# Kernel optimization log

Hardware: AMD Instinct MI355X
Metric: run time of the kernel (lower is better)

## Reference

```python
import jax, jax.numpy as jnp
import numpy as np

N = 20000
E = 100000
IN_CH = 512
OUT_CH = 256
HID = 2 * OUT_CH          # 512
CAT = 5 * HID             # 2560
BN_EPS = 1e-5


def _sage(x, src, dst, w_edge, Wl, Wr, b):
    """PyG SAGEConv (mean aggr): lin_l(mean_{j->i} x_j) + lin_r(x_i).
    w_edge: per-edge float weight (0/1 mask); messages flow src -> dst."""
    msg = x[src] * w_edge[:, None]                              # [E, F]
    s = jax.ops.segment_sum(msg, dst, num_segments=N)           # [N, F]
    cnt = jax.ops.segment_sum(w_edge, dst, num_segments=N)      # [N]
    mean = s / jnp.maximum(cnt, 1.0)[:, None]
    return mean @ Wl.T + x @ Wr.T + b


def setup_inputs() -> dict:
    key = jax.random.key(0)
    ks = jax.random.split(key, 12)
    x = jax.random.normal(ks[0], (N, IN_CH), dtype=jnp.float32)
    edge_index = jax.random.randint(ks[1], (2, E), 0, N, dtype=jnp.int64)
    edge_attr = jax.random.randint(ks[2], (E,), 0, 5, dtype=jnp.int64)
    sc = 1.0 / np.sqrt(IN_CH)
    Wl5 = jax.random.uniform(ks[3], (5, HID, IN_CH), jnp.float32, -sc, sc)
    Wr5 = jax.random.uniform(ks[4], (5, HID, IN_CH), jnp.float32, -sc, sc)
    bl5 = jnp.zeros((5, HID), jnp.float32)
    sc2 = 1.0 / np.sqrt(CAT)
    Wmu_l = jax.random.uniform(ks[5], (OUT_CH, CAT), jnp.float32, -sc2, sc2)
    Wmu_r = jax.random.uniform(ks[6], (OUT_CH, CAT), jnp.float32, -sc2, sc2)
    bmu = jnp.zeros((OUT_CH,), jnp.float32)
    Wlv_l = jax.random.uniform(ks[7], (OUT_CH, CAT), jnp.float32, -sc2, sc2)
    Wlv_r = jax.random.uniform(ks[8], (OUT_CH, CAT), jnp.float32, -sc2, sc2)
    blv = jnp.zeros((OUT_CH,), jnp.float32)
    gamma = jnp.ones((CAT,), jnp.float32)
    beta = jnp.zeros((CAT,), jnp.float32)
    run_mean = jax.random.normal(ks[9], (CAT,), jnp.float32) * 0.1
    run_var = jnp.abs(jax.random.normal(ks[10], (CAT,), jnp.float32)) + 1.0
    return {"x": x, "edge_index": edge_index, "edge_attr": edge_attr,
            "Wl5": Wl5, "Wr5": Wr5, "bl5": bl5,
            "Wmu_l": Wmu_l, "Wmu_r": Wmu_r, "bmu": bmu,
            "Wlv_l": Wlv_l, "Wlv_r": Wlv_r, "blv": blv,
            "gamma": gamma, "beta": beta,
            "run_mean": run_mean, "run_var": run_var}


def reference(x, edge_index, edge_attr, Wl5, Wr5, bl5,
              Wmu_l, Wmu_r, bmu, Wlv_l, Wlv_r, blv,
              gamma, beta, run_mean, run_var):
    # eval mode: all dropouts are identity, BatchNorm uses running stats.
    src, dst = edge_index[0], edge_index[1]
    # 5 relation branches: mask edges by relation id instead of nonzero slicing
    branches = []
    for k in range(5):
        w = (edge_attr == k).astype(x.dtype)                    # [E]
        h = _sage(x, src, dst, w, Wl5[k], Wr5[k], bl5[k])       # [N, HID]
        branches.append(jax.nn.relu(h))
    h = jnp.concatenate(branches, axis=1)                       # [N, CAT]
    # BatchNorm1d (eval)
    h = (h - run_mean) * jax.lax.rsqrt(run_var + BN_EPS) * gamma + beta
    ones = jnp.ones((E,), x.dtype)
    mu = _sage(h, src, dst, ones, Wmu_l, Wmu_r, bmu)            # [N, OUT_CH]
    logvar = _sage(h, src, dst, ones, Wlv_l, Wlv_r, blv)        # [N, OUT_CH]
    return (mu, logvar)
```

## Files before the change

kernel.cpp:

```cpp
#include <hip/hip_runtime.h>
#include <stdint.h>

#define INCH 512
#define HIDW 512
#define CATW 2560
#define OUTW 256
#define BN_EPS 1e-5f
#define TS 1024

typedef __bf16 bf16x8 __attribute__((ext_vector_type(8)));
typedef float f32x4 __attribute__((ext_vector_type(4)));

__device__ __forceinline__ unsigned short f2bf(float f) {
  union { float f; unsigned u; } v; v.f = f;
  unsigned r = v.u + 0x7FFFu + ((v.u >> 16) & 1u);
  return (unsigned short)(r >> 16);
}

__device__ __forceinline__ float bf2f(unsigned short u) {
  union { unsigned u; float f; } v; v.u = ((unsigned)u) << 16; return v.f;
}

__device__ __forceinline__ void pack4(unsigned short* dst, float a, float b, float c, float d) {
  unsigned lo = (unsigned)f2bf(a) | ((unsigned)f2bf(b) << 16);
  unsigned hi = (unsigned)f2bf(c) | ((unsigned)f2bf(d) << 16);
  *reinterpret_cast<uint2*>(dst) = make_uint2(lo, hi);
}


__global__ void cvt_bf16_kernel(const float* __restrict__ in, unsigned short* __restrict__ out, int n4) {
  int g = blockIdx.x * blockDim.x + threadIdx.x;
  if (g >= n4) return;
  int base = g * 4;
  float4 v = *reinterpret_cast<const float4*>(in + base);
  pack4(out + base, v.x, v.y, v.z, v.w);
}

__global__ void pack_w1p_kernel(const float* __restrict__ Wl, const float* __restrict__ Wr,
                                unsigned short* __restrict__ out) {
  int g = blockIdx.x * blockDim.x + threadIdx.x;
  if (g >= 5 * 128 * 512) return;
  int z = g >> 16;
  int rem = g & 65535;
  int c = rem >> 9;
  int j = rem & 511;
  int kk = c * 8;
  const float* src = (kk < 512) ? (Wl + ((size_t)(z * 512 + j)) * 512 + kk)
                                : (Wr + ((size_t)(z * 512 + j)) * 512 + (kk - 512));
  float4 a = *reinterpret_cast<const float4*>(src);
  float4 b = *reinterpret_cast<const float4*>(src + 4);
  pack4(out + (size_t)g * 8, a.x, a.y, a.z, a.w);
  pack4(out + (size_t)g * 8 + 4, b.x, b.y, b.z, b.w);
}

__global__ void pack_w23p_kernel(const float* __restrict__ Wmu_l, const float* __restrict__ Wlv_l,
                                 const float* __restrict__ Wmu_r, const float* __restrict__ Wlv_r,
                                 unsigned short* __restrict__ out) {
  int g = blockIdx.x * blockDim.x + threadIdx.x;
  if (g >= 320 * 1024) return;
  int c = g >> 10;
  int j = g & 1023;
  const float* row;
  if (j < 256)       row = Wmu_l + (size_t)j * CATW;
  else if (j < 512)  row = Wlv_l + (size_t)(j - 256) * CATW;
  else if (j < 768)  row = Wmu_r + (size_t)(j - 512) * CATW;
  else               row = Wlv_r + (size_t)(j - 768) * CATW;
  const float* src = row + c * 8;
  float4 a = *reinterpret_cast<const float4*>(src);
  float4 b = *reinterpret_cast<const float4*>(src + 4);
  pack4(out + (size_t)g * 8, a.x, a.y, a.z, a.w);
  pack4(out + (size_t)g * 8 + 4, b.x, b.y, b.z, b.w);
}


__global__ void hist_kernel(const int* __restrict__ ei, const int* __restrict__ ea,
                            int* __restrict__ cnt, int E) {
  int e = blockIdx.x * 256 + threadIdx.x;
  if (e >= E) return;
  atomicAdd(&cnt[ei[E + e] * 5 + ea[e]], 1);
}

__global__ void scan1_kernel(const int* __restrict__ in, int* __restrict__ out,
                             int* __restrict__ bsum, int n) {
  __shared__ int lds[256];
  int t = threadIdx.x;
  int base = blockIdx.x * TS + t * 4;
  int4 v = make_int4(0, 0, 0, 0);
  if (base + 3 < n) v = *reinterpret_cast<const int4*>(in + base);
  else {
    if (base < n) v.x = in[base];
    if (base + 1 < n) v.y = in[base + 1];
    if (base + 2 < n) v.z = in[base + 2];
    if (base + 3 < n) v.w = in[base + 3];
  }
  int s = v.x + v.y + v.z + v.w;
  lds[t] = s;
  __syncthreads();
  for (int o = 1; o < 256; o <<= 1) {
    int a = (t >= o) ? lds[t - o] : 0;
    __syncthreads();
    lds[t] += a;
    __syncthreads();
  }
  int excl = lds[t] - s;
  if (t == 255) bsum[blockIdx.x] = lds[255];
  int e0 = excl, e1 = e0 + v.x, e2 = e1 + v.y, e3 = e2 + v.z;
  if (base < n) out[base] = e0;
  if (base + 1 < n) out[base + 1] = e1;
  if (base + 2 < n) out[base + 2] = e2;
  if (base + 3 < n) out[base + 3] = e3;
}

__global__ void scan2_kernel(int* __restrict__ bsum, int nb) {
  __shared__ int lds[128];
  int t = threadIdx.x;
  int v = (t < nb) ? bsum[t] : 0;
  lds[t] = v;
  __syncthreads();
  for (int o = 1; o < 128; o <<= 1) {
    int a = (t >= o) ? lds[t - o] : 0;
    __syncthreads();
    lds[t] += a;
    __syncthreads();
  }
  if (t < nb) bsum[t] = lds[t] - v;
}

__global__ void scan3_kernel(int* __restrict__ out, const int* __restrict__ bsum,
                             int n, int total) {
  int g = blockIdx.x * 256 + threadIdx.x;
  if (g == 0) out[n] = total;
  int base = g * 4;
  if (base >= n) return;
  int add = bsum[base / TS];
  if (base + 3 < n) {
    int4 v = *reinterpret_cast<int4*>(out + base);
    v.x += add; v.y += add; v.z += add; v.w += add;
    *reinterpret_cast<int4*>(out + base) = v;
  } else {
    for (int q = 0; q < 4 && base + q < n; ++q) out[base + q] += add;
  }
}

__global__ void fill_kernel(const int* __restrict__ ei, const int* __restrict__ ea,
                            const int* __restrict__ offs, int* __restrict__ fillc,
                            int* __restrict__ perm, int E) {
  int e = blockIdx.x * 256 + threadIdx.x;
  if (e >= E) return;
  int key = ei[E + e] * 5 + ea[e];
  int p = atomicAdd(&fillc[key], 1);
  perm[offs[key] + p] = ei[e];
}


__global__ void gather1_kernel(const unsigned short* __restrict__ xb, const int* __restrict__ offs,
                               const int* __restrict__ perm, unsigned short* __restrict__ meanb5) {
  int i = blockIdx.x;
  int k = blockIdx.y;
  int t = threadIdx.x;
  int b0 = offs[i * 5 + k], b1 = offs[i * 5 + k + 1];
  float a0 = 0.f, a1 = 0.f, a2 = 0.f, a3 = 0.f;
  for (int e = b0; e < b1; ++e) {
    int s = perm[e];
    ushort4 v = reinterpret_cast<const ushort4*>(xb + (size_t)s * 512)[t];
    a0 += bf2f(v.x); a1 += bf2f(v.y); a2 += bf2f(v.z); a3 += bf2f(v.w);
  }
  float inv = (b1 > b0) ? 1.0f / (float)(b1 - b0) : 0.0f;
  pack4(meanb5 + (size_t)i * CATW + k * 512 + t * 4, a0 * inv, a1 * inv, a2 * inv, a3 * inv);
}

__global__ void gather2_kernel(const float* __restrict__ z, const int* __restrict__ offs,
                               const int* __restrict__ perm, float* __restrict__ mean2) {
  int i = blockIdx.x;
  int t = threadIdx.x;
  int b0 = offs[i * 5], b1 = offs[i * 5 + 5];
  float4 acc = make_float4(0.f, 0.f, 0.f, 0.f);
  for (int e = b0; e < b1; ++e) {
    int s = perm[e];
    float4 v = reinterpret_cast<const float4*>(z + (size_t)s * 512)[t];
    acc.x += v.x; acc.y += v.y; acc.z += v.z; acc.w += v.w;
  }
  float inv = (b1 > b0) ? 1.0f / (float)(b1 - b0) : 1.0f;
  reinterpret_cast<float4*>(mean2 + (size_t)i * 512)[t] =
      make_float4(acc.x * inv, acc.y * inv, acc.z * inv, acc.w * inv);
}

__global__ void add_kernel(float* __restrict__ dout, const float* __restrict__ mean2,
                           const float* __restrict__ bmu, const float* __restrict__ blv,
                           int M, int n4) {
  int g = blockIdx.x * 256 + threadIdx.x;
  if (g >= n4) return;
  int base = g * 4;
  int i = base >> 9;
  int c = base & 511;
  float4 m2 = *reinterpret_cast<const float4*>(mean2 + (size_t)i * 512 + c);
  int cc = c & 255;
  float* op;
  const float* bp;
  if (c < 256) { op = dout + (size_t)i * OUTW + cc; bp = bmu + cc; }
  else         { op = dout + (size_t)M * OUTW + (size_t)i * OUTW + cc; bp = blv + cc; }
  float4 y = *reinterpret_cast<float4*>(op);
  float4 b = *reinterpret_cast<const float4*>(bp);
  y.x += m2.x + b.x; y.y += m2.y + b.y; y.z += m2.z + b.z; y.w += m2.w + b.w;
  *reinterpret_cast<float4*>(op) = y;
}

template<int MODE>
__global__ __launch_bounds__(256, 3)
void gemm_kernel(const unsigned short* __restrict__ A,
                 const unsigned short* __restrict__ A2,
                 const unsigned short* __restrict__ B,
                 unsigned short* __restrict__ hOut,
                 float* __restrict__ fOut,
                 float* __restrict__ fOut2,
                 const float* __restrict__ p0,
                 const float* __restrict__ p1,
                 const float* __restrict__ p2,
                 const float* __restrict__ p3,
                 const float* __restrict__ p4,
                 int M)
{
  constexpr int KTOT = (MODE == 0) ? (2 * INCH) : CATW;
  constexpr int KT = KTOT / 32;
  constexpr int NBLK = (MODE == 0) ? 4 : 8;
  constexpr int NC = (MODE == 0) ? 512 : 1024;

  const int nwg = gridDim.x;
  const int o = blockIdx.x;
  const int q = nwg >> 3, r = nwg & 7;
  const int xcd = o & 7;
  const int wg = (xcd < r ? xcd * (q + 1) : r * (q + 1) + (xcd - r) * q) + (o >> 3);
  const int rowBase = (wg / NBLK) * 128;
  const int nBase = (wg % NBLK) * 128;
  const int z = (MODE == 0) ? blockIdx.z : 0;
  const unsigned short* BpF = (MODE == 0) ? (B + (size_t)z * 524288) : B;

  __shared__ unsigned short As[4][4096];

  const int tid = threadIdx.x;
  const int lane = tid & 63;
  const int wv = tid >> 6;
  const int wr = wv >> 1, wc = wv & 1;
  const int lr = lane & 15, kg = lane >> 4;

  const int srow0 = (wv * 2) * 16 + (lane >> 2);
  const int srow1 = srow0 + 16;
  const int kswz = (((lane & 3) ^ ((lane >> 4) & 3)) * 8);
  int gar0 = rowBase + srow0; if (gar0 >= M) gar0 = M - 1;
  int gar1 = rowBase + srow1; if (gar1 >= M) gar1 = M - 1;

  int aslot[4];
#pragma unroll
  for (int m = 0; m < 4; ++m) {
    const int ar = wr * 64 + m * 16 + lr;
    aslot[m] = ar * 32 + ((kg ^ ((lr >> 2) & 3)) * 8);
  }

  size_t bjoff[4];
#pragma unroll
  for (int n = 0; n < 4; ++n)
    bjoff[n] = (size_t)(nBase + wc * 64 + n * 16 + lr) * 8;

  f32x4 acc[4][4] = {};

  auto stageA = [&](int slot, int kt) {
    const int kk0 = kt * 32;
    const unsigned short *a0p, *a1p;
    if (MODE == 0) {
      if (kk0 < INCH) {
        a0p = A + (size_t)gar0 * CATW + z * 512 + kk0 + kswz;
        a1p = A + (size_t)gar1 * CATW + z * 512 + kk0 + kswz;
      } else {
        a0p = A2 + (size_t)gar0 * INCH + (kk0 - INCH) + kswz;
        a1p = A2 + (size_t)gar1 * INCH + (kk0 - INCH) + kswz;
      }
    } else {
      a0p = A + (size_t)gar0 * KTOT + kk0 + kswz;
      a1p = A + (size_t)gar1 * KTOT + kk0 + kswz;
    }
    __builtin_amdgcn_global_load_lds((const void*)a0p, (void*)&As[slot][(wv * 2) * 512], 16, 0, 0);
    __builtin_amdgcn_global_load_lds((const void*)a1p, (void*)&As[slot][(wv * 2 + 1) * 512], 16, 0, 0);
  };

  auto loadB = [&](int kt, bf16x8 (&dst)[4]) {
    const size_t cbase = (size_t)((kt << 2) + kg) * NC * 8;
#pragma unroll
    for (int n = 0; n < 4; ++n)
      dst[n] = *reinterpret_cast<const bf16x8*>(BpF + cbase + bjoff[n]);
  };

  auto step = [&](int t, const bf16x8 (&bcur)[4], bf16x8 (&bnxt)[4]) {
    const int slot = t & 3;
    bf16x8 af[4];
#pragma unroll
    for (int m = 0; m < 4; ++m)
      af[m] = *reinterpret_cast<const bf16x8*>(&As[slot][aslot[m]]);
    if (t + 1 < KT) loadB(t + 1, bnxt);
    if (t + 3 < KT) stageA((t + 3) & 3, t + 3);
    __builtin_amdgcn_sched_barrier(0);
    __builtin_amdgcn_s_setprio(1);
#pragma unroll
    for (int m = 0; m < 4; ++m)
#pragma unroll
      for (int n = 0; n < 4; ++n)
        acc[m][n] = __builtin_amdgcn_mfma_f32_16x16x32_bf16(af[m], bcur[n], acc[m][n], 0, 0, 0);
    __builtin_amdgcn_s_setprio(0);
    __builtin_amdgcn_sched_barrier(0);
    __builtin_amdgcn_s_barrier();
    __builtin_amdgcn_sched_barrier(0);
  };

  bf16x8 bP[4], bQ[4];
  stageA(0, 0);
  stageA(1, 1);
  stageA(2, 2);
  __builtin_amdgcn_sched_barrier(0);
  loadB(0, bP);
  __builtin_amdgcn_sched_barrier(0);
  asm volatile("s_waitcnt vmcnt(8)" ::: "memory");
  __builtin_amdgcn_s_barrier();
  __builtin_amdgcn_sched_barrier(0);

  for (int t = 0; t < KT; t += 2) {
    step(t, bP, bQ);
    step(t + 1, bQ, bP);
  }

#pragma unroll
  for (int n = 0; n < 4; ++n) {
    const int j = nBase + wc * 64 + n * 16 + lr;
    if (MODE == 0) {
      const int ch = z * 512 + j;
      const float bias = p0[ch];
      const float scale = rsqrtf(p2[ch] + BN_EPS) * p3[ch];
      const float rm = p1[ch], be = p4[ch];
#pragma unroll
      for (int m = 0; m < 4; ++m) {
        const int ib = rowBase + wr * 64 + m * 16 + kg * 4;
#pragma unroll
        for (int rr = 0; rr < 4; ++rr) {
          const int i = ib + rr;
          if (i < M) {
            float v = acc[m][n][rr] + bias;
            v = fmaxf(v, 0.0f);
            v = (v - rm) * scale + be;
            hOut[(size_t)i * CATW + ch] = f2bf(v);
          }
        }
      }
    } else {
#pragma unroll
      for (int m = 0; m < 4; ++m) {
        const int ib = rowBase + wr * 64 + m * 16 + kg * 4;
#pragma unroll
        for (int rr = 0; rr < 4; ++rr) {
          const int i = ib + rr;
          if (i < M) {
            const float v = acc[m][n][rr];
            if (j < 512) {
              fOut[(size_t)i * 512 + j] = v;
            } else {
              const int jj = j - 512;
              size_t o2 = (jj < OUTW) ? ((size_t)i * OUTW + jj)
                                      : ((size_t)M * OUTW + (size_t)i * OUTW + (jj - OUTW));
              fOut2[o2] = v;
            }
          }
        }
      }
    }
  }
}


extern "C" void kernel_launch(void* const* d_in, const int* in_sizes, int n_in,
                              void* d_out, int out_size, void* d_ws, size_t ws_size,
                              hipStream_t stream) {
  const float* x     = (const float*)d_in[0];
  const int*   ei    = (const int*)d_in[1];
  const int*   ea    = (const int*)d_in[2];
  const float* Wl5   = (const float*)d_in[3];
  const float* Wr5   = (const float*)d_in[4];
  const float* bl5   = (const float*)d_in[5];
  const float* Wmu_l = (const float*)d_in[6];
  const float* Wmu_r = (const float*)d_in[7];
  const float* bmu   = (const float*)d_in[8];
  const float* Wlv_l = (const float*)d_in[9];
  const float* Wlv_r = (const float*)d_in[10];
  const float* blv   = (const float*)d_in[11];
  const float* gamma = (const float*)d_in[12];
  const float* beta  = (const float*)d_in[13];
  const float* rmean = (const float*)d_in[14];
  const float* rvar  = (const float*)d_in[15];
  (void)n_in; (void)out_size;

  const int N = in_sizes[0] / INCH;
  const int E = in_sizes[2];
  const int NKEY = N * 5;

  char* ws = (char*)d_ws;
  size_t off = 0;
  auto take = [&](size_t bytes) { char* p = ws + off; off += (bytes + 255) & ~(size_t)255; return p; };
  unsigned short* hb = (unsigned short*)take((size_t)N * CATW * 2);
  char* U = take((size_t)N * CATW * 2);
  unsigned short* xb = (unsigned short*)take((size_t)N * 512 * 2);
  unsigned short* w1p  = (unsigned short*)take((size_t)5 * 128 * 512 * 8 * 2);
  unsigned short* w23p = (unsigned short*)take((size_t)320 * 1024 * 8 * 2);
  int* cntk  = (int*)take((size_t)NKEY * 4);
  int* offs  = (int*)take((size_t)(NKEY + 1) * 4);
  int* fillc = (int*)take((size_t)NKEY * 4);
  int* perm  = (int*)take((size_t)E * 4);
  int* bsum  = (int*)take(256 * 4);
  if (off > ws_size) return;

  unsigned short* meanb5 = (unsigned short*)U;
  float* zbuf  = (float*)U;
  float* mean2 = (float*)(U + (size_t)N * 512 * 4);

  cvt_bf16_kernel<<<dim3((N * INCH / 4 + 255) / 256), 256, 0, stream>>>(x, xb, N * INCH / 4);
  pack_w1p_kernel<<<dim3((5 * 128 * 512 + 255) / 256), 256, 0, stream>>>(Wl5, Wr5, w1p);
  pack_w23p_kernel<<<dim3((320 * 1024 + 255) / 256), 256, 0, stream>>>(Wmu_l, Wlv_l, Wmu_r, Wlv_r, w23p);

  hipMemsetAsync(cntk, 0, (size_t)NKEY * 4, stream);
  hipMemsetAsync(fillc, 0, (size_t)NKEY * 4, stream);
  hist_kernel<<<dim3((E + 255) / 256), 256, 0, stream>>>(ei, ea, cntk, E);
  const int nb = (NKEY + TS - 1) / TS;
  scan1_kernel<<<dim3(nb), 256, 0, stream>>>(cntk, offs, bsum, NKEY);
  scan2_kernel<<<dim3(1), 128, 0, stream>>>(bsum, nb);
  scan3_kernel<<<dim3((NKEY / 4 + 255) / 256 + 1), 256, 0, stream>>>(offs, bsum, NKEY, E);
  fill_kernel<<<dim3((E + 255) / 256), 256, 0, stream>>>(ei, ea, offs, fillc, perm, E);

  gather1_kernel<<<dim3(N, 5), 128, 0, stream>>>(xb, offs, perm, meanb5);
  const int mblk = (N + 127) / 128;
  gemm_kernel<0><<<dim3(mblk * 4, 1, 5), 256, 0, stream>>>(
      meanb5, xb, w1p, hb, nullptr, nullptr,
      bl5, rmean, rvar, gamma, beta, N);

  gemm_kernel<1><<<dim3(mblk * 8, 1, 1), 256, 0, stream>>>(
      hb, nullptr, w23p, nullptr, zbuf, (float*)d_out,
      nullptr, nullptr, nullptr, nullptr, nullptr, N);

  gather2_kernel<<<dim3(N), 128, 0, stream>>>(zbuf, offs, perm, mean2);

  add_kernel<<<dim3((N * 512 / 4 + 255) / 256), 256, 0, stream>>>(
      (float*)d_out, mean2, bmu, blv, N, N * 512 / 4);
}
```

Measured before the change: 435.8 us.

## Stage GEMM epilogues through LDS for coalesced stores and fuse add into gather2

Both GEMM epilogues now write accumulator tiles into shared memory (swizzled for the bf16 path) and then emit 16-byte vectorized, row-contiguous global stores, replacing scattered 2- and 4-byte stores. The second gather kernel now adds the neighbor mean plus bias directly into the output, which removes the separate add kernel and the intermediate mean2 buffer round-trip. The cost is extra LDS traffic and barriers in the epilogue, plus reuse of the A staging buffer, which must be large enough for 128x128 bf16 or 128x64 fp32 tiles.

```diff
diff --git a/kernel.cpp b/kernel.cpp
--- a/kernel.cpp
+++ b/kernel.cpp
@@ -170,7 +170,9 @@
 }
 
 __global__ void gather2_kernel(const float* __restrict__ z, const int* __restrict__ offs,
-                               const int* __restrict__ perm, float* __restrict__ mean2) {
+                               const int* __restrict__ perm, float* __restrict__ dout,
+                               const float* __restrict__ bmu, const float* __restrict__ blv,
+                               int M) {
   int i = blockIdx.x;
   int t = threadIdx.x;
   int b0 = offs[i * 5], b1 = offs[i * 5 + 5];
@@ -181,27 +183,15 @@
     acc.x += v.x; acc.y += v.y; acc.z += v.z; acc.w += v.w;
   }
   float inv = (b1 > b0) ? 1.0f / (float)(b1 - b0) : 1.0f;
-  reinterpret_cast<float4*>(mean2 + (size_t)i * 512)[t] =
-      make_float4(acc.x * inv, acc.y * inv, acc.z * inv, acc.w * inv);
-}
-
-__global__ void add_kernel(float* __restrict__ dout, const float* __restrict__ mean2,
-                           const float* __restrict__ bmu, const float* __restrict__ blv,
-                           int M, int n4) {
-  int g = blockIdx.x * 256 + threadIdx.x;
-  if (g >= n4) return;
-  int base = g * 4;
-  int i = base >> 9;
-  int c = base & 511;
-  float4 m2 = *reinterpret_cast<const float4*>(mean2 + (size_t)i * 512 + c);
-  int cc = c & 255;
+  int c = t * 4;
   float* op;
   const float* bp;
-  if (c < 256) { op = dout + (size_t)i * OUTW + cc; bp = bmu + cc; }
-  else         { op = dout + (size_t)M * OUTW + (size_t)i * OUTW + cc; bp = blv + cc; }
+  if (c < 256) { op = dout + (size_t)i * OUTW + c; bp = bmu + c; }
+  else         { op = dout + (size_t)M * OUTW + (size_t)i * OUTW + (c - 256); bp = blv + (c - 256); }
   float4 y = *reinterpret_cast<float4*>(op);
   float4 b = *reinterpret_cast<const float4*>(bp);
-  y.x += m2.x + b.x; y.y += m2.y + b.y; y.z += m2.z + b.z; y.w += m2.w + b.w;
+  y.x += acc.x * inv + b.x; y.y += acc.y * inv + b.y;
+  y.z += acc.z * inv + b.z; y.w += acc.w * inv + b.w;
   *reinterpret_cast<float4*>(op) = y;
 }
 
@@ -326,46 +316,76 @@
     step(t + 1, bQ, bP);
   }
 
-#pragma unroll
-  for (int n = 0; n < 4; ++n) {
-    const int j = nBase + wc * 64 + n * 16 + lr;
-    if (MODE == 0) {
-      const int ch = z * 512 + j;
+  if (MODE == 0) {
+    unsigned short* lds16 = &As[0][0];
+#pragma unroll
+    for (int n = 0; n < 4; ++n) {
+      const int j = wc * 64 + n * 16 + lr;
+      const int ch = z * 512 + nBase + j;
       const float bias = p0[ch];
       const float scale = rsqrtf(p2[ch] + BN_EPS) * p3[ch];
       const float rm = p1[ch], be = p4[ch];
 #pragma unroll
-      for (int m = 0; m < 4; ++m) {
-        const int ib = rowBase + wr * 64 + m * 16 + kg * 4;
+      for (int m = 0; m < 4; ++m)
 #pragma unroll
         for (int rr = 0; rr < 4; ++rr) {
-          const int i = ib + rr;
-          if (i < M) {
-            float v = acc[m][n][rr] + bias;
-            v = fmaxf(v, 0.0f);
-            v = (v - rm) * scale + be;
-            hOut[(size_t)i * CATW + ch] = f2bf(v);
-          }
+          const int row = wr * 64 + m * 16 + kg * 4 + rr;
+          float v = acc[m][n][rr] + bias;
+          v = fmaxf(v, 0.0f);
+          v = (v - rm) * scale + be;
+          lds16[row * 128 + (j ^ ((row & 7) << 3))] = f2bf(v);
+        }
+    }
+    __syncthreads();
+    const int trow = tid >> 4;
+    const int cb = tid & 15;
+#pragma unroll
+    for (int p = 0; p < 8; ++p) {
+      const int row = p * 16 + trow;
+      const int i = rowBase + row;
+      if (i < M) {
+        const int scb = cb ^ (row & 7);
+        uint4 v = *reinterpret_cast<const uint4*>(&lds16[row * 128 + scb * 8]);
+        *reinterpret_cast<uint4*>(&hOut[(size_t)i * CATW + z * 512 + nBase + cb * 8]) = v;
+      }
+    }
+  } else {
+    float* ldsf = reinterpret_cast<float*>(&As[0][0]);
+#pragma unroll
+    for (int hp = 0; hp < 2; ++hp) {
+      __syncthreads();
+      if (wc == hp) {
+#pragma unroll
+        for (int n = 0; n < 4; ++n) {
+          const int jl = n * 16 + lr;
+#pragma unroll
+          for (int m = 0; m < 4; ++m)
+#pragma unroll
+            for (int rr = 0; rr < 4; ++rr) {
+              const int row = wr * 64 + m * 16 + kg * 4 + rr;
+              ldsf[row * 64 + jl] = acc[m][n][rr];
+            }
         }
       }
-    } else {
-#pragma unroll
-      for (int m = 0; m < 4; ++m) {
-        const int ib = rowBase + wr * 64 + m * 16 + kg * 4;
-#pragma unroll
-        for (int rr = 0; rr < 4; ++rr) {
-          const int i = ib + rr;
-          if (i < M) {
-            const float v = acc[m][n][rr];
-            if (j < 512) {
-              fOut[(size_t)i * 512 + j] = v;
-            } else {
-              const int jj = j - 512;
-              size_t o2 = (jj < OUTW) ? ((size_t)i * OUTW + jj)
-                                      : ((size_t)M * OUTW + (size_t)i * OUTW + (jj - OUTW));
-              fOut2[o2] = v;
-            }
+      __syncthreads();
+      const int trow = tid >> 4, cb = tid & 15;
+      const int jbase = nBase + hp * 64;
+#pragma unroll
+      for (int p = 0; p < 8; ++p) {
+        const int row = p * 16 + trow;
+        const int i = rowBase + row;
+        if (i < M) {
+          float4 v = *reinterpret_cast<const float4*>(&ldsf[row * 64 + cb * 4]);
+          const int j = jbase + cb * 4;
+          float* dst;
+          if (j < 512) {
+            dst = fOut + (size_t)i * 512 + j;
+          } else {
+            const int jj = j - 512;
+            dst = (jj < OUTW) ? (fOut2 + (size_t)i * OUTW + jj)
+                              : (fOut2 + (size_t)M * OUTW + (size_t)i * OUTW + (jj - OUTW));
           }
+          *reinterpret_cast<float4*>(dst) = v;
         }
       }
     }
@@ -415,7 +435,6 @@
 
   unsigned short* meanb5 = (unsigned short*)U;
   float* zbuf  = (float*)U;
-  float* mean2 = (float*)(U + (size_t)N * 512 * 4);
 
   cvt_bf16_kernel<<<dim3((N * INCH / 4 + 255) / 256), 256, 0, stream>>>(x, xb, N * INCH / 4);
   pack_w1p_kernel<<<dim3((5 * 128 * 512 + 255) / 256), 256, 0, stream>>>(Wl5, Wr5, w1p);
@@ -440,8 +459,5 @@
       hb, nullptr, w23p, nullptr, zbuf, (float*)d_out,
       nullptr, nullptr, nullptr, nullptr, nullptr, N);
 
-  gather2_kernel<<<dim3(N), 128, 0, stream>>>(zbuf, offs, perm, mean2);
-
-  add_kernel<<<dim3((N * 512 / 4 + 255) / 256), 256, 0, stream>>>(
-      (float*)d_out, mean2, bmu, blv, N, N * 512 / 4);
-}
+  gather2_kernel<<<dim3(N), 128, 0, stream>>>(zbuf, offs, perm, (float*)d_out, bmu, blv, N);
+}
```

New measurement: 368.9 us. -15.4%, faster.
